# Kernel optimization log

Hardware: AMD Instinct MI355X
Metric: run time of the kernel (lower is better)

The kernel has to match this reference:

```python
import jax, jax.numpy as jnp
import numpy as np

K = 20

def knn_idx(x, k):
    # x: [N, D] -> indices of k nearest neighbors (excluding self), [N, k]
    sq = jnp.sum(x * x, axis=-1)
    d = sq[:, None] + sq[None, :] - 2.0 * (x @ x.T)
    n = x.shape[0]
    d = d.at[jnp.arange(n), jnp.arange(n)].set(jnp.inf)
    _, idx = jax.lax.top_k(-d, k)
    return idx

def edge_conv(x, W, b, k):
    # DynamicEdgeConv: feat = [x_i, x_j - x_i] -> MLP -> max over neighbors
    idx = knn_idx(x, k)                      # [N, k]
    xj = x[idx]                              # [N, k, D]
    xi = jnp.broadcast_to(x[:, None, :], xj.shape)
    feat = jnp.concatenate([xi, xj - xi], axis=-1)   # [N, k, 2D]
    h = jax.nn.relu(feat @ W + b)            # [N, k, C]
    return jnp.max(h, axis=1)                # [N, C]

def dilate_flat(x, W, b, k):
    # DilateFlatEdgeConv: flat morphological dilation (max over kNN) + MLP
    idx = knn_idx(x, k)
    dil = jnp.max(x[idx], axis=1)            # [N, C]
    return jax.nn.relu(dil @ W + b)

def setup_inputs() -> dict:
    key = jax.random.key(0)
    ks = jax.random.split(key, 12)
    N, C, NC = 8192, 64, 16
    s = 0.05
    return {
        "x": jax.random.normal(ks[0], (N, 3), dtype=jnp.float32),
        "W1": jax.random.normal(ks[1], (6, C), dtype=jnp.float32) * s,
        "b1": jnp.zeros((C,), jnp.float32),
        "Wd1": jax.random.normal(ks[2], (C, C), dtype=jnp.float32) * s,
        "bd1": jnp.zeros((C,), jnp.float32),
        "Wd2": jax.random.normal(ks[3], (C, C), dtype=jnp.float32) * s,
        "bd2": jnp.zeros((C,), jnp.float32),
        "Wd3": jax.random.normal(ks[4], (C, C), dtype=jnp.float32) * s,
        "bd3": jnp.zeros((C,), jnp.float32),
        "Wl": jax.random.normal(ks[5], (3 * C, 1024), dtype=jnp.float32) * s,
        "bl": jnp.zeros((1024,), jnp.float32),
        "Wm1": jax.random.normal(ks[6], (1024, 256), dtype=jnp.float32) * s,
        "bm1": jnp.zeros((256,), jnp.float32),
        "Wm2": jax.random.normal(ks[7], (256, 128), dtype=jnp.float32) * s,
        "bm2": jnp.zeros((128,), jnp.float32),
        "Wm3": jax.random.normal(ks[8], (128, NC), dtype=jnp.float32) * s,
        "bm3": jnp.zeros((NC,), jnp.float32),
    }

def reference(x, W1, b1, Wd1, bd1, Wd2, bd2, Wd3, bd3, Wl, bl, Wm1, bm1, Wm2, bm2, Wm3, bm3):
    x_feat = edge_conv(x, W1, b1, K)          # [N, 64]
    x1 = dilate_flat(x_feat, Wd1, bd1, K) - x_feat
    x2 = dilate_flat(x1, Wd2, bd2, K) - x1
    x3 = dilate_flat(x2, Wd3, bd3, K) - x2
    h = jax.nn.relu(jnp.concatenate([x1, x2, x3], axis=1) @ Wl + bl)  # [N, 1024]
    h = jax.nn.relu(h @ Wm1 + bm1)            # dropout is identity at eval
    h = jax.nn.relu(h @ Wm2 + bm2)
    logits = h @ Wm3 + bm3
    return jax.nn.log_softmax(logits, axis=-1)
```

## Files before the change

### kernel.cpp

```cpp
#include <hip/hip_runtime.h>
#include <math.h>

#define NPTS 8192
#define KNN 20
#define KSEL 8
#define CAPD3 256
#define CAP64 512
#define LCAP 2048

typedef __attribute__((ext_vector_type(8))) short bf16x8;
typedef __attribute__((ext_vector_type(16))) float f32x16;

__device__ __forceinline__ uint32_t fkey(float v) {
  uint32_t b = __float_as_uint(v);
  return b ^ ((uint32_t)((int)b >> 31) | 0x80000000u);
}
__device__ __forceinline__ float unkey(uint32_t k) {
  uint32_t b = (k & 0x80000000u) ? (k ^ 0x80000000u) : ~k;
  return __uint_as_float(b);
}
__device__ __forceinline__ ushort f2bf(float v) {
  uint32_t u = __float_as_uint(v);
  u += 0x7FFFu + ((u >> 16) & 1u);
  return (ushort)(u >> 16);
}
__device__ __forceinline__ float bf2f(ushort h) {
  return __uint_as_float(((uint32_t)h) << 16);
}

__device__ __forceinline__ void insert8k(uint32_t (&d)[KSEL], uint32_t key) {
#pragma unroll
  for (int r = 0; r < KSEL; ++r) {
    uint32_t nd = min(d[r], key);
    key = max(d[r], key);
    d[r] = nd;
  }
}

__global__ void sqnorm_kernel(const float* __restrict__ x, int ldx, int D,
                              float* __restrict__ sq,
                              unsigned int* __restrict__ nmax2u) {
  int i = blockIdx.x * blockDim.x + threadIdx.x;
  if (i >= NPTS) return;
  const float* xr = x + (size_t)i * ldx;
  float s = 0.f;
  for (int d = 0; d < D; ++d) { float v = xr[d]; s += v * v; }
  sq[i] = s;
  atomicMax(nmax2u, __float_as_uint(s));
}

__global__ __launch_bounds__(256) void tobf16_kernel(
    const float* __restrict__ x, int ldx, ushort* __restrict__ xh,
    ushort* __restrict__ xl) {
  const int i = blockIdx.x * 256 + threadIdx.x;
  const int row = (i * 8) >> 6, col = (i * 8) & 63;
  const float* src = &x[(size_t)row * ldx + col];
  ushort oh[8], ol[8];
#pragma unroll
  for (int e = 0; e < 8; ++e) {
    float v = src[e];
    ushort h = f2bf(v);
    oh[e] = h;
    ol[e] = f2bf(v - bf2f(h));
  }
  *(ushort4*)&xh[(size_t)row * 64 + col] =
      make_ushort4(oh[0], oh[1], oh[2], oh[3]);
  *(ushort4*)&xh[(size_t)row * 64 + col + 4] =
      make_ushort4(oh[4], oh[5], oh[6], oh[7]);
  *(ushort4*)&xl[(size_t)row * 64 + col] =
      make_ushort4(ol[0], ol[1], ol[2], ol[3]);
  *(ushort4*)&xl[(size_t)row * 64 + col + 4] =
      make_ushort4(ol[4], ol[5], ol[6], ol[7]);
}

#define WRITE_S(QR, BASE)                                                   \
  {                                                                         \
    const int cc = (4 * bg) & 31;                                           \
    const int jbase = cb + (QR)*32 + cc;                                    \
    _Pragma("unroll") for (int u = 0; u < 8; ++u) {                         \
      const int row = 4 * am + (u & 3) + 64 * (u >> 2);                     \
      const int gq = qb * 128 + row;                                        \
      const int sw = ((row & 7) ^ ((row >> 2) & 7)) << 2;                   \
      uint32_t k0 = fkey(fmaf(-2.f, acc[u][(BASE) + 0], sc[(BASE) + 0]));   \
      uint32_t k1 = fkey(fmaf(-2.f, acc[u][(BASE) + 1], sc[(BASE) + 1]));   \
      uint32_t k2 = fkey(fmaf(-2.f, acc[u][(BASE) + 2], sc[(BASE) + 2]));   \
      uint32_t k3 = fkey(fmaf(-2.f, acc[u][(BASE) + 3], sc[(BASE) + 3]));   \
      if (jbase + 0 == gq) k0 = 0xFFFFFFFFu;                                \
      if (jbase + 1 == gq) k1 = 0xFFFFFFFFu;                                \
      if (jbase + 2 == gq) k2 = 0xFFFFFFFFu;                                \
      if (jbase + 3 == gq) k3 = 0xFFFFFFFFu;                                \
      *(uint4*)&S[row * 32 + (cc ^ sw)] = make_uint4(k0, k1, k2, k3);       \
    }                                                                       \
  }

#define COMMIT_CS()                                                         \
  {                                                                         \
    Cs[(ck + 0) * 128 + cn] = p0.x;  Cs[(ck + 1) * 128 + cn] = p0.y;        \
    Cs[(ck + 2) * 128 + cn] = p0.z;  Cs[(ck + 3) * 128 + cn] = p0.w;        \
    Cs[(ck + 4) * 128 + cn] = p1.x;  Cs[(ck + 5) * 128 + cn] = p1.y;        \
    Cs[(ck + 6) * 128 + cn] = p1.z;  Cs[(ck + 7) * 128 + cn] = p1.w;        \
    Cs[(ck + 8) * 128 + cn] = p2.x;  Cs[(ck + 9) * 128 + cn] = p2.y;        \
    Cs[(ck + 10) * 128 + cn] = p2.z; Cs[(ck + 11) * 128 + cn] = p2.w;       \
    Cs[(ck + 12) * 128 + cn] = p3.x; Cs[(ck + 13) * 128 + cn] = p3.y;       \
    Cs[(ck + 14) * 128 + cn] = p3.z; Cs[(ck + 15) * 128 + cn] = p3.w;       \
  }

#define ISSUE_CS(BASEROW, KOFF)                                             \
  {                                                                         \
    const float* src_ = &x[(size_t)((BASEROW) + cn) * LDX + (KOFF) + ck];   \
    p0 = *(const float4*)&src_[0];                                          \
    p1 = *(const float4*)&src_[4];                                          \
    p2 = *(const float4*)&src_[8];                                          \
    p3 = *(const float4*)&src_[12];                                         \
  }

template <int LDX>
__global__ __launch_bounds__(256, 2) void knn_gemm_kernel(
    const float* __restrict__ x, const float* __restrict__ sq,
    uint32_t* __restrict__ pk) {
  __shared__ float Qs[64 * 128];
  __shared__ uint32_t CsS[32 * 128];
  float* const Cs = (float*)CsS;
  uint32_t* const S = CsS;
  const int t = threadIdx.x;
  const int qb = blockIdx.x;
  const int ch = blockIdx.y;
  const int am = t & 15;
  const int bg = (t >> 4) & 15;
  const int cn = t & 127;
  const int ck = (t >> 7) * 16;

  {
    const int q = t & 127;
    const int k0 = (t >> 7) * 32;
    const float* src = &x[(size_t)(qb * 128 + q) * LDX + k0];
#pragma unroll
    for (int c = 0; c < 8; ++c) {
      float4 v = *(const float4*)&src[c * 4];
      Qs[(k0 + c * 4 + 0) * 128 + q] = v.x;
      Qs[(k0 + c * 4 + 1) * 128 + q] = v.y;
      Qs[(k0 + c * 4 + 2) * 128 + q] = v.z;
      Qs[(k0 + c * 4 + 3) * 128 + q] = v.w;
    }
  }

  const int selq = t & 127, part = t >> 7;
  uint32_t dreg[KSEL];
#pragma unroll
  for (int r = 0; r < KSEL; ++r) dreg[r] = 0xFFFFFFFFu;

  float4 p0, p1, p2, p3;
  ISSUE_CS(ch * 256, 0)

#pragma unroll 1
  for (int tile = 0; tile < 2; ++tile) {
    const int cb = ch * 256 + tile * 128;
    float acc[8][8] = {};
#pragma unroll
    for (int kh = 0; kh < 2; ++kh) {
      __syncthreads();
      COMMIT_CS()
      if (kh == 0) {
        ISSUE_CS(cb, 32)
      } else if (tile == 0) {
        ISSUE_CS(cb + 128, 0)
      }
      __syncthreads();
#pragma unroll 4
      for (int k2 = 0; k2 < 32; ++k2) {
        const int k = kh * 32 + k2;
        float4 A0 = *(const float4*)&Qs[k * 128 + 4 * am];
        float4 A1 = *(const float4*)&Qs[k * 128 + 4 * am + 64];
        float4 B0 = *(const float4*)&Cs[k2 * 128 + 4 * bg];
        float4 B1 = *(const float4*)&Cs[k2 * 128 + 4 * bg + 64];
        float a[8] = {A0.x, A0.y, A0.z, A0.w, A1.x, A1.y, A1.z, A1.w};
        float b[8] = {B0.x, B0.y, B0.z, B0.w, B1.x, B1.y, B1.z, B1.w};
#pragma unroll
        for (int u = 0; u < 8; ++u)
#pragma unroll
          for (int v = 0; v < 8; ++v) acc[u][v] = fmaf(a[u], b[v], acc[u][v]);
      }
    }
    float4 s0 = *(const float4*)&sq[cb + 4 * bg];
    float4 s1 = *(const float4*)&sq[cb + 4 * bg + 64];
    float sc[8] = {s0.x, s0.y, s0.z, s0.w, s1.x, s1.y, s1.z, s1.w};

    const int qlow = bg >> 3;
    for (int qr = 0; qr < 4; ++qr) {
      __syncthreads();
      if (qr == qlow) WRITE_S(qr, 0);
      if (qr == 2 + qlow) WRITE_S(qr, 4);
      __syncthreads();
      const int swr = ((selq & 7) ^ ((selq >> 2) & 7)) << 2;
#pragma unroll
      for (int g_ = 0; g_ < 4; ++g_) {
        const int cc = part * 16 + g_ * 4;
        uint4 sv = *(const uint4*)&S[selq * 32 + (cc ^ swr)];
        uint32_t kv[4] = {sv.x, sv.y, sv.z, sv.w};
#pragma unroll
        for (int e = 0; e < 4; ++e) {
          if (kv[e] < dreg[KSEL - 1]) insert8k(dreg, kv[e]);
        }
      }
    }
  }
  const int l = ch * 2 + part;
  uint32_t* pkq = pk + ((size_t)l * NPTS + (qb * 128 + selq)) * KSEL;
#pragma unroll
  for (int r = 0; r < KSEL; ++r) pkq[r] = dreg[r];
}

__global__ __launch_bounds__(256) void knn_mergeT_kernel(
    const uint32_t* __restrict__ pk, const float* __restrict__ sq,
    const float* __restrict__ nmax2, float* __restrict__ Tf, float mscale) {
  __shared__ uint32_t sk[16][16][KSEL];
  const int t = threadIdx.x;
  const int ql = t >> 4;
  const int l = t & 15;
  const int q = blockIdx.x * 16 + ql;
  const uint32_t* pkq = pk + ((size_t)l * NPTS + q) * KSEL;
#pragma unroll
  for (int r = 0; r < KSEL; ++r) sk[ql][l][r] = pkq[r];
  __syncthreads();
  int ptr = 0;
  uint32_t k = 0;
#pragma unroll 1
  for (int s = 0; s < KNN; ++s) {
    k = (ptr < KSEL) ? sk[ql][l][ptr] : 0xFFFFFFFFu;
    int src = l;
#pragma unroll
    for (int off = 8; off >= 1; off >>= 1) {
      uint32_t ok = __shfl_xor(k, off, 16);
      int osrc = __shfl_xor(src, off, 16);
      bool take = (ok < k) || (ok == k && osrc < src);
      k = take ? ok : k;
      src = take ? osrc : src;
    }
    if (l == src) ptr++;
  }
  if (l == 0) Tf[q] = unkey(k) + mscale * sqrtf(sq[q] * nmax2[0]);
}

__global__ __launch_bounds__(256, 2) void knn_recover_mfma_kernel(
    const ushort* __restrict__ xh, const ushort* __restrict__ xl,
    const float* __restrict__ sq, const float* __restrict__ Tf,
    uint32_t* __restrict__ cnt, int* __restrict__ cj) {
  __shared__ uint32_t nsurv;
  __shared__ uint2 surv[LCAP];
  const int t = threadIdx.x;
  const int w = t >> 6, l = t & 63;
  const int q0 = blockIdx.x * 128 + (w >> 1) * 64;
  const int c0 = blockIdx.y * 128 + (w & 1) * 64;
  const int lr = l & 31;
  const int ko = (l >> 5) * 8;
  const int rowbase = (l >> 5) * 4;

  if (t == 0) nsurv = 0;

  float tq[2][16];
#pragma unroll
  for (int rt = 0; rt < 2; ++rt)
#pragma unroll
    for (int r = 0; r < 16; ++r)
      tq[rt][r] = Tf[q0 + rt * 32 + (r & 3) + 8 * (r >> 2) + rowbase];

  f32x16 acc[2][2] = {};
#pragma unroll
  for (int kk = 0; kk < 4; ++kk) {
    bf16x8 Ah[2], Al[2], Bh[2], Bl[2];
#pragma unroll
    for (int rt = 0; rt < 2; ++rt) {
      const size_t off = (size_t)(q0 + rt * 32 + lr) * 64 + kk * 16 + ko;
      Ah[rt] = *(const bf16x8*)&xh[off];
      Al[rt] = *(const bf16x8*)&xl[off];
    }
#pragma unroll
    for (int ct = 0; ct < 2; ++ct) {
      const size_t off = (size_t)(c0 + ct * 32 + lr) * 64 + kk * 16 + ko;
      Bh[ct] = *(const bf16x8*)&xh[off];
      Bl[ct] = *(const bf16x8*)&xl[off];
    }
#pragma unroll
    for (int rt = 0; rt < 2; ++rt)
#pragma unroll
      for (int ct = 0; ct < 2; ++ct) {
        acc[rt][ct] = __builtin_amdgcn_mfma_f32_32x32x16_bf16(
            Ah[rt], Bh[ct], acc[rt][ct], 0, 0, 0);
        acc[rt][ct] = __builtin_amdgcn_mfma_f32_32x32x16_bf16(
            Ah[rt], Bl[ct], acc[rt][ct], 0, 0, 0);
        acc[rt][ct] = __builtin_amdgcn_mfma_f32_32x32x16_bf16(
            Al[rt], Bh[ct], acc[rt][ct], 0, 0, 0);
      }
  }
  __syncthreads();

#pragma unroll
  for (int ct = 0; ct < 2; ++ct) {
    const int j = c0 + ct * 32 + lr;
    const float sqj = sq[j];
#pragma unroll
    for (int rt = 0; rt < 2; ++rt) {
#pragma unroll
      for (int r = 0; r < 16; ++r) {
        const int gq = q0 + rt * 32 + (r & 3) + 8 * (r >> 2) + rowbase;
        float d = fmaf(-2.f, acc[rt][ct][r], sqj);
        if (j != gq && d <= tq[rt][r]) {
          uint32_t idx = atomicAdd(&nsurv, 1u);
          if (idx < (uint32_t)LCAP) {
            surv[idx] = make_uint2((uint32_t)gq, (uint32_t)j);
          } else {
            uint32_t slot = atomicAdd(&cnt[gq], 1u);
            if (slot < (uint32_t)CAP64) cj[(size_t)gq * CAP64 + slot] = j;
          }
        }
      }
    }
  }
  __syncthreads();
  const uint32_t nv = min(nsurv, (uint32_t)LCAP);
#pragma unroll 1
  for (uint32_t i = t; i < nv; i += 256) {
    uint2 e = surv[i];
    uint32_t slot = atomicAdd(&cnt[e.x], 1u);
    if (slot < (uint32_t)CAP64) cj[(size_t)e.x * CAP64 + slot] = (int)e.y;
  }
}

template <int LDX>
__global__ __launch_bounds__(256) void knn_final64_kernel(
    const float* __restrict__ x, const float* __restrict__ sq,
    const uint32_t* __restrict__ cnt, const int* __restrict__ cj,
    int* __restrict__ idx_out) {
  __shared__ float xqs[4][64];
  const int t = threadIdx.x, w = t >> 6, l = t & 63;
  const int q = blockIdx.x * 4 + w;
  if (l < 16)
    *(float4*)&xqs[w][l * 4] = *(const float4*)&x[(size_t)q * LDX + l * 4];
  __syncthreads();
  const int n = (int)min(cnt[q], (uint32_t)CAP64);
  uint32_t ks[8]; int js[8];
#pragma unroll
  for (int r = 0; r < 8; ++r) { ks[r] = 0xFFFFFFFFu; js[r] = 0x7fffffff; }
#pragma unroll 1
  for (int it = 0; it < 8; ++it) {
    const int c = l + it * 64;
    if (c < n) {
      const int j = cj[(size_t)q * CAP64 + c];
      const float* xj = &x[(size_t)j * LDX];
      float dot = 0.f;
#pragma unroll
      for (int e = 0; e < 16; ++e) {
        float4 a = *(const float4*)&xj[e * 4];
        float4 b = *(const float4*)&xqs[w][e * 4];
        dot = fmaf(a.x, b.x, dot);
        dot = fmaf(a.y, b.y, dot);
        dot = fmaf(a.z, b.z, dot);
        dot = fmaf(a.w, b.w, dot);
      }
      float d = fmaf(-2.f, dot, sq[j]);
      uint32_t ck = fkey(d);
      int ci = j;
#pragma unroll
      for (int r = 0; r < 8; ++r) {
        bool sw = (ck < ks[r]) || (ck == ks[r] && ci < js[r]);
        uint32_t ok = ks[r]; int oj = js[r];
        ks[r] = sw ? ck : ok; js[r] = sw ? ci : oj;
        ck = sw ? ok : ck; ci = sw ? oj : ci;
      }
    }
  }
#pragma unroll 1
  for (int s = 0; s < KNN; ++s) {
    uint32_t mk = ks[0];
    int mj = js[0];
#pragma unroll
    for (int off = 32; off >= 1; off >>= 1) {
      uint32_t ok = __shfl_xor(mk, off, 64);
      int oj = __shfl_xor(mj, off, 64);
      bool take = (ok < mk) || (ok == mk && oj < mj);
      mk = take ? ok : mk;
      mj = take ? oj : mj;
    }
    if (ks[0] == mk && js[0] == mj) {
#pragma unroll
      for (int r = 0; r < 7; ++r) { ks[r] = ks[r + 1]; js[r] = js[r + 1]; }
      ks[7] = 0xFFFFFFFFu; js[7] = 0x7fffffff;
    }
    if (l == 0) idx_out[(size_t)q * KNN + s] = mj;
  }
}

__global__ __launch_bounds__(256) void knn_d3k_kernel(
    const float* __restrict__ x, const float* __restrict__ sq,
    uint32_t* __restrict__ pk) {
  __shared__ float4 Ct[128];
  const int t = threadIdx.x;
  const int q = blockIdx.x * 256 + t;
  const int ch = blockIdx.y;
  const int cb = ch * 128;
  if (t < 128)
    Ct[t] = make_float4(x[(cb + t) * 3], x[(cb + t) * 3 + 1],
                        x[(cb + t) * 3 + 2], sq[cb + t]);
  const float xi0 = x[q * 3], xi1 = x[q * 3 + 1], xi2 = x[q * 3 + 2];
  uint32_t dreg[KSEL];
#pragma unroll
  for (int r = 0; r < KSEL; ++r) dreg[r] = 0xFFFFFFFFu;
  __syncthreads();
#pragma unroll 1
  for (int c = 0; c < 128; ++c) {
    float4 cv = Ct[c];
    int j = cb + c;
    float val = fmaf(-2.f, xi0 * cv.x + xi1 * cv.y + xi2 * cv.z, cv.w);
    uint32_t key = fkey(val);
    if (j != q && key < dreg[KSEL - 1]) insert8k(dreg, key);
  }
  uint32_t* pkq = pk + ((size_t)ch * NPTS + q) * KSEL;
#pragma unroll
  for (int r = 0; r < KSEL; ++r) pkq[r] = dreg[r];
}

__global__ __launch_bounds__(256) void knn_d3_recover_kernel(
    const float* __restrict__ x, const float* __restrict__ sq,
    const float* __restrict__ Tf, uint32_t* __restrict__ cnt,
    uint32_t* __restrict__ cd, int* __restrict__ cj) {
  __shared__ float4 Ct[256];
  const int t = threadIdx.x;
  const int q = blockIdx.x * 256 + t;
  const int ch = blockIdx.y;
  const int cb = ch * 256;
  Ct[t] = make_float4(x[(cb + t) * 3], x[(cb + t) * 3 + 1],
                      x[(cb + t) * 3 + 2], sq[cb + t]);
  const float xi0 = x[q * 3], xi1 = x[q * 3 + 1], xi2 = x[q * 3 + 2];
  const float Tq = Tf[q];
  __syncthreads();
#pragma unroll 1
  for (int c = 0; c < 256; ++c) {
    float4 cv = Ct[c];
    int j = cb + c;
    float val = fmaf(-2.f, xi0 * cv.x + xi1 * cv.y + xi2 * cv.z, cv.w);
    if (j != q && val <= Tq) {
      uint32_t slot = atomicAdd(&cnt[q], 1u);
      if (slot < (uint32_t)CAPD3) {
        cd[(size_t)q * CAPD3 + slot] = fkey(val);
        cj[(size_t)q * CAPD3 + slot] = j;
      }
    }
  }
}

#define CSWAP(ka, ja, kb, jb)                                   \
  {                                                             \
    bool sw = (kb < ka) || (kb == ka && jb < ja);               \
    uint32_t tk = sw ? kb : ka; int tj = sw ? jb : ja;          \
    kb = sw ? ka : kb; jb = sw ? ja : jb;                       \
    ka = tk; ja = tj;                                           \
  }

__global__ __launch_bounds__(256) void knn_final_d3_kernel(
    const uint32_t* __restrict__ cnt, const uint32_t* __restrict__ cd,
    const int* __restrict__ cj, int* __restrict__ idx_out) {
  const int t = threadIdx.x;
  const int w = t >> 6;
  const int l = t & 63;
  const int q = blockIdx.x * 4 + w;
  const int n = (int)min(cnt[q], (uint32_t)CAPD3);
  uint32_t k0 = 0xFFFFFFFFu, k1 = 0xFFFFFFFFu, k2 = 0xFFFFFFFFu,
           k3 = 0xFFFFFFFFu;
  int j0 = 0x7fffffff, j1 = 0x7fffffff, j2 = 0x7fffffff, j3 = 0x7fffffff;
  if (l < n) { k0 = cd[(size_t)q * CAPD3 + l]; j0 = cj[(size_t)q * CAPD3 + l]; }
  if (l + 64 < n) { k1 = cd[(size_t)q * CAPD3 + l + 64]; j1 = cj[(size_t)q * CAPD3 + l + 64]; }
  if (l + 128 < n) { k2 = cd[(size_t)q * CAPD3 + l + 128]; j2 = cj[(size_t)q * CAPD3 + l + 128]; }
  if (l + 192 < n) { k3 = cd[(size_t)q * CAPD3 + l + 192]; j3 = cj[(size_t)q * CAPD3 + l + 192]; }
  CSWAP(k0, j0, k1, j1); CSWAP(k2, j2, k3, j3);
  CSWAP(k0, j0, k2, j2); CSWAP(k1, j1, k3, j3);
  CSWAP(k1, j1, k2, j2);
#pragma unroll 1
  for (int s = 0; s < KNN; ++s) {
    uint32_t mk = k0;
    int mj = j0;
#pragma unroll
    for (int off = 32; off >= 1; off >>= 1) {
      uint32_t ok = __shfl_xor(mk, off, 64);
      int oj = __shfl_xor(mj, off, 64);
      bool take = (ok < mk) || (ok == mk && oj < mj);
      mk = take ? ok : mk;
      mj = take ? oj : mj;
    }
    if (k0 == mk && j0 == mj) {
      k0 = k1; j0 = j1; k1 = k2; j1 = j2; k2 = k3; j2 = j3;
      k3 = 0xFFFFFFFFu; j3 = 0x7fffffff;
    }
    if (l == 0) idx_out[(size_t)q * KNN + s] = mj;
  }
}

__global__ __launch_bounds__(256) void edgeconv_kernel(
    const float* __restrict__ x, const int* __restrict__ idx,
    const float* __restrict__ W1, const float* __restrict__ b1,
    float* __restrict__ out) {
  const int i = blockIdx.x * 4 + (threadIdx.x >> 6);
  const int c = threadIdx.x & 63;
  float w0 = W1[c], w1 = W1[64 + c], w2 = W1[128 + c];
  float w3 = W1[192 + c], w4 = W1[256 + c], w5 = W1[320 + c];
  float xi0 = x[3 * i], xi1 = x[3 * i + 1], xi2 = x[3 * i + 2];
  float base = b1[c] + xi0 * w0 + xi1 * w1 + xi2 * w2;
  float m = -INFINITY;
#pragma unroll
  for (int k = 0; k < KNN; ++k) {
    int j = idx[i * KNN + k];
    float d0 = x[3 * j] - xi0, d1 = x[3 * j + 1] - xi1, d2 = x[3 * j + 2] - xi2;
    float h = base + d0 * w3 + d1 * w4 + d2 * w5;
    m = fmaxf(m, fmaxf(h, 0.f));
  }
  out[(size_t)i * 64 + c] = m;
}

__global__ __launch_bounds__(256) void dilate_kernel(
    const float* __restrict__ xin, int ldin, const int* __restrict__ idx,
    const float* __restrict__ W, const float* __restrict__ bias,
    float* __restrict__ out, int ldout) {
  const int g = threadIdx.x >> 6;
  const int i = blockIdx.x * 4 + g;
  const int c = threadIdx.x & 63;
  __shared__ float dil[4][64];
  float m = -INFINITY;
#pragma unroll
  for (int k = 0; k < KNN; ++k) {
    int j = idx[i * KNN + k];
    m = fmaxf(m, xin[(size_t)j * ldin + c]);
  }
  dil[g][c] = m;
  __syncthreads();
  float acc = bias[c];
#pragma unroll
  for (int d = 0; d < 64; ++d) acc = fmaf(dil[g][d], W[d * 64 + c], acc);
  out[(size_t)i * ldout + c] = fmaxf(acc, 0.f) - xin[(size_t)i * ldin + c];
}

template <int BN>
__global__ __launch_bounds__(256) void gemm128_kernel(
    const float* __restrict__ A, int K, int ldA, const float* __restrict__ W,
    int N, const float* __restrict__ bias, float* __restrict__ C, int ldC,
    int relu) {
  constexpr int VN = BN / 16;
  __shared__ float As[16 * 128];
  __shared__ float Bs[16 * BN];
  const int t = threadIdx.x;
  const int bn = blockIdx.x * BN;
  const int bm = blockIdx.y * 128;
  const int am = t & 15;
  const int bg = (t >> 4) & 15;
  float acc[8][VN] = {};

  for (int k0 = 0; k0 < K; k0 += 16) {
    __syncthreads();
    {
      const int m = t & 127;
      const int ka = (t >> 7) * 8;
      const float* src = &A[(size_t)(bm + m) * ldA + k0 + ka];
      float4 v0 = *(const float4*)&src[0];
      float4 v1 = *(const float4*)&src[4];
      As[(ka + 0) * 128 + m] = v0.x;
      As[(ka + 1) * 128 + m] = v0.y;
      As[(ka + 2) * 128 + m] = v0.z;
      As[(ka + 3) * 128 + m] = v0.w;
      As[(ka + 4) * 128 + m] = v1.x;
      As[(ka + 5) * 128 + m] = v1.y;
      As[(ka + 6) * 128 + m] = v1.z;
      As[(ka + 7) * 128 + m] = v1.w;
    }
    if constexpr (BN == 128) {
      const int kb = t >> 4;
      const int n8 = (t & 15) * 8;
      const float* src = &W[(size_t)(k0 + kb) * N + bn + n8];
      float4 v0 = *(const float4*)&src[0];
      float4 v1 = *(const float4*)&src[4];
      *(float4*)&Bs[kb * BN + n8] = v0;
      *(float4*)&Bs[kb * BN + n8 + 4] = v1;
    } else {
      const int kb = t >> 4;
      const int n4 = (t & 15) * 4;
      const float* src = &W[(size_t)(k0 + kb) * N + bn + n4];
      *(float4*)&Bs[kb * BN + n4] = *(const float4*)&src[0];
    }
    __syncthreads();
#pragma unroll
    for (int k = 0; k < 16; ++k) {
      float4 A0 = *(const float4*)&As[k * 128 + 4 * am];
      float4 A1 = *(const float4*)&As[k * 128 + 4 * am + 64];
      float a[8] = {A0.x, A0.y, A0.z, A0.w, A1.x, A1.y, A1.z, A1.w};
      float b[VN];
      float4 B0 = *(const float4*)&Bs[k * BN + 4 * bg];
      b[0] = B0.x; b[1] = B0.y; b[2] = B0.z; b[3] = B0.w;
      if constexpr (BN == 128) {
        float4 B1 = *(const float4*)&Bs[k * BN + 4 * bg + 64];
        b[4] = B1.x; b[5] = B1.y; b[6] = B1.z; b[7] = B1.w;
      }
#pragma unroll
      for (int u = 0; u < 8; ++u)
#pragma unroll
        for (int v = 0; v < VN; ++v) acc[u][v] = fmaf(a[u], b[v], acc[u][v]);
    }
  }
#pragma unroll
  for (int u = 0; u < 8; ++u) {
    const int m = bm + 4 * am + (u & 3) + 64 * (u >> 2);
#pragma unroll
    for (int vq = 0; vq < VN / 4; ++vq) {
      const int n = bn + 4 * bg + 64 * vq;
      float4 o;
      float* po = (float*)&o;
#pragma unroll
      for (int e = 0; e < 4; ++e) {
        float val = acc[u][vq * 4 + e] + bias[n + e];
        po[e] = relu ? fmaxf(val, 0.f) : val;
      }
      *(float4*)&C[(size_t)m * ldC + n] = o;
    }
  }
}

__global__ __launch_bounds__(256) void final_kernel(
    const float* __restrict__ h3, const float* __restrict__ Wm3,
    const float* __restrict__ bm3, float* __restrict__ out) {
  __shared__ float hs[16][132];
  const int tid = threadIdx.x;
  const int r = tid >> 4, c = tid & 15;
  const int row0 = blockIdx.x * 16;
#pragma unroll
  for (int l = tid; l < 2048; l += 256)
    hs[l >> 7][l & 127] = h3[(size_t)row0 * 128 + l];
  __syncthreads();
  float acc = bm3[c];
#pragma unroll
  for (int d = 0; d < 128; ++d) acc = fmaf(hs[r][d], Wm3[d * 16 + c], acc);
  float mx = acc;
#pragma unroll
  for (int o = 8; o >= 1; o >>= 1) mx = fmaxf(mx, __shfl_xor(mx, o, 16));
  float e = expf(acc - mx);
  float s = e;
#pragma unroll
  for (int o = 8; o >= 1; o >>= 1) s += __shfl_xor(s, o, 16);
  out[(size_t)(row0 + r) * 16 + c] = (acc - mx) - logf(s);
}

extern "C" void kernel_launch(void* const* d_in, const int* in_sizes, int n_in,
                              void* d_out, int out_size, void* d_ws,
                              size_t ws_size, hipStream_t stream) {
  const float* x = (const float*)d_in[0];
  const float* W1 = (const float*)d_in[1];
  const float* b1 = (const float*)d_in[2];
  const float* Wd1 = (const float*)d_in[3];
  const float* bd1 = (const float*)d_in[4];
  const float* Wd2 = (const float*)d_in[5];
  const float* bd2 = (const float*)d_in[6];
  const float* Wd3 = (const float*)d_in[7];
  const float* bd3 = (const float*)d_in[8];
  const float* Wl = (const float*)d_in[9];
  const float* bl = (const float*)d_in[10];
  const float* Wm1 = (const float*)d_in[11];
  const float* bm1 = (const float*)d_in[12];
  const float* Wm2 = (const float*)d_in[13];
  const float* bm2 = (const float*)d_in[14];
  const float* Wm3 = (const float*)d_in[15];
  const float* bm3 = (const float*)d_in[16];
  float* out = (float*)d_out;

  char* ws = (char*)d_ws;
  float* sq = (float*)(ws + 0);
  int* idxA = (int*)(ws + 32768);
  float* xfeat = (float*)(ws + 1343488);
  float* xcat = (float*)(ws + 3440640);
  float* h1 = (float*)(ws + 9732096);
  float* h2 = (float*)(ws + 43286528);
  float* h3 = (float*)(ws + 51675136);
  float* x1 = xcat;
  float* x2 = xcat + 64;
  float* x3 = xcat + 128;
  uint32_t* pk = (uint32_t*)(ws + 9732096);
  uint32_t* cdD3 = (uint32_t*)(ws + 13926400);
  int* cjD3 = (int*)(ws + 22315008);
  float* Tf = (float*)(ws + 30703616);
  uint32_t* cnt = (uint32_t*)(ws + 30736384);
  unsigned int* nmax2u = (unsigned int*)(ws + 30769152);
  float* nmax2f = (float*)nmax2u;
  int* cj64 = (int*)(ws + 30769216);
  ushort* xh = (ushort*)(ws + 47546432);
  ushort* xl = (ushort*)(ws + 48595008);

  hipMemsetAsync(cnt, 0, 32768 + 64, stream);
  sqnorm_kernel<<<32, 256, 0, stream>>>(x, 3, 3, sq, nmax2u);
  knn_d3k_kernel<<<dim3(32, 16), 256, 0, stream>>>(x, sq, pk);
  knn_mergeT_kernel<<<NPTS / 16, 256, 0, stream>>>(pk, sq, nmax2f, Tf, 0.f);
  knn_d3_recover_kernel<<<dim3(32, 32), 256, 0, stream>>>(x, sq, Tf, cnt,
                                                          cdD3, cjD3);
  knn_final_d3_kernel<<<NPTS / 4, 256, 0, stream>>>(cnt, cdD3, cjD3, idxA);
  edgeconv_kernel<<<NPTS / 4, 256, 0, stream>>>(x, idxA, W1, b1, xfeat);

#define KNN64_PASS(XIN, LDX)                                                  \
  hipMemsetAsync(cnt, 0, 32768 + 64, stream);                                 \
  sqnorm_kernel<<<32, 256, 0, stream>>>(XIN, LDX, 64, sq, nmax2u);            \
  tobf16_kernel<<<256, 256, 0, stream>>>(XIN, LDX, xh, xl);                   \
  knn_gemm_kernel<LDX><<<dim3(64, 8), 256, 0, stream>>>(XIN, sq, pk);         \
  knn_mergeT_kernel<<<NPTS / 16, 256, 0, stream>>>(pk, sq, nmax2f, Tf,        \
                                                   1e-4f);                    \
  knn_recover_mfma_kernel<<<dim3(64, 64), 256, 0, stream>>>(xh, xl, sq, Tf,   \
                                                            cnt, cj64);       \
  knn_final64_kernel<LDX><<<NPTS / 4, 256, 0, stream>>>(XIN, sq, cnt, cj64,   \
                                                        idxA);

  KNN64_PASS(xfeat, 64)
  dilate_kernel<<<NPTS / 4, 256, 0, stream>>>(xfeat, 64, idxA, Wd1, bd1, x1,
                                              192);
  KNN64_PASS(x1, 192)
  dilate_kernel<<<NPTS / 4, 256, 0, stream>>>(x1, 192, idxA, Wd2, bd2, x2,
                                              192);
  KNN64_PASS(x2, 192)
  dilate_kernel<<<NPTS / 4, 256, 0, stream>>>(x2, 192, idxA, Wd3, bd3, x3,
                                              192);
#undef KNN64_PASS

  gemm128_kernel<128><<<dim3(1024 / 128, NPTS / 128), 256, 0, stream>>>(
      xcat, 192, 192, Wl, 1024, bl, h1, 1024, 1);
  gemm128_kernel<64><<<dim3(256 / 64, NPTS / 128), 256, 0, stream>>>(
      h1, 1024, 1024, Wm1, 256, bm1, h2, 256, 1);
  gemm128_kernel<64><<<dim3(128 / 64, NPTS / 128), 256, 0, stream>>>(
      h2, 256, 256, Wm2, 128, bm2, h3, 128, 1);
  final_kernel<<<NPTS / 16, 256, 0, stream>>>(h3, Wm3, bm3, out);
}
```

Baseline: 1.013 ms.

## Stage kNN recover survivors in LDS and prefetch GEMM tiles into registers

The d3 recover kernel now collects threshold survivors in a shared-memory list through an LDS atomic, then flushes them to global per-query buckets after a barrier. This replaces per-hit global atomics issued inside the divergent scan loop; entries that overflow the shared list still take the old global path. Separately, the fp32 GEMM kernel now loads the next K-tile's A and B values into registers while the current tile is computed, overlapping global loads with FMA work at the cost of extra registers.

```diff
diff --git a/kernel.cpp b/kernel.cpp
--- a/kernel.cpp
+++ b/kernel.cpp
@@ -424,10 +424,13 @@
     const float* __restrict__ Tf, uint32_t* __restrict__ cnt,
     uint32_t* __restrict__ cd, int* __restrict__ cj) {
   __shared__ float4 Ct[256];
+  __shared__ uint32_t nsurv;
+  __shared__ uint2 surv[LCAP];
   const int t = threadIdx.x;
-  const int q = blockIdx.x * 256 + t;
-  const int ch = blockIdx.y;
-  const int cb = ch * 256;
+  const int q0 = blockIdx.x * 256;
+  const int q = q0 + t;
+  const int cb = blockIdx.y * 256;
+  if (t == 0) nsurv = 0;
   Ct[t] = make_float4(x[(cb + t) * 3], x[(cb + t) * 3 + 1],
                       x[(cb + t) * 3 + 2], sq[cb + t]);
   const float xi0 = x[q * 3], xi1 = x[q * 3 + 1], xi2 = x[q * 3 + 2];
@@ -439,11 +442,29 @@
     int j = cb + c;
     float val = fmaf(-2.f, xi0 * cv.x + xi1 * cv.y + xi2 * cv.z, cv.w);
     if (j != q && val <= Tq) {
-      uint32_t slot = atomicAdd(&cnt[q], 1u);
-      if (slot < (uint32_t)CAPD3) {
-        cd[(size_t)q * CAPD3 + slot] = fkey(val);
-        cj[(size_t)q * CAPD3 + slot] = j;
-      }
+      uint32_t idx = atomicAdd(&nsurv, 1u);
+      if (idx < (uint32_t)LCAP) {
+        surv[idx] = make_uint2(fkey(val), ((uint32_t)t << 16) | (uint32_t)j);
+      } else {
+        uint32_t slot = atomicAdd(&cnt[q], 1u);
+        if (slot < (uint32_t)CAPD3) {
+          cd[(size_t)q * CAPD3 + slot] = fkey(val);
+          cj[(size_t)q * CAPD3 + slot] = j;
+        }
+      }
+    }
+  }
+  __syncthreads();
+  const uint32_t nv = min(nsurv, (uint32_t)LCAP);
+#pragma unroll 1
+  for (uint32_t i = t; i < nv; i += 256) {
+    uint2 e = surv[i];
+    const int qq = q0 + (int)(e.y >> 16);
+    const int jj = (int)(e.y & 0xFFFFu);
+    uint32_t slot = atomicAdd(&cnt[qq], 1u);
+    if (slot < (uint32_t)CAPD3) {
+      cd[(size_t)qq * CAPD3 + slot] = e.x;
+      cj[(size_t)qq * CAPD3 + slot] = jj;
     }
   }
 }
@@ -550,38 +571,41 @@
   const int bm = blockIdx.y * 128;
   const int am = t & 15;
   const int bg = (t >> 4) & 15;
+  const int m_ = t & 127;
+  const int ka = (t >> 7) * 8;
+  const int kb = t >> 4;
+  const int nb = (t & 15) * (BN == 128 ? 8 : 4);
   float acc[8][VN] = {};
+  float4 av0, av1, bv0, bv1;
+
+  {
+    const float* srcA = &A[(size_t)(bm + m_) * ldA + ka];
+    av0 = *(const float4*)&srcA[0];
+    av1 = *(const float4*)&srcA[4];
+    const float* srcB = &W[(size_t)kb * N + bn + nb];
+    bv0 = *(const float4*)&srcB[0];
+    if constexpr (BN == 128) bv1 = *(const float4*)&srcB[4];
+  }
 
   for (int k0 = 0; k0 < K; k0 += 16) {
     __syncthreads();
-    {
-      const int m = t & 127;
-      const int ka = (t >> 7) * 8;
-      const float* src = &A[(size_t)(bm + m) * ldA + k0 + ka];
-      float4 v0 = *(const float4*)&src[0];
-      float4 v1 = *(const float4*)&src[4];
-      As[(ka + 0) * 128 + m] = v0.x;
-      As[(ka + 1) * 128 + m] = v0.y;
-      As[(ka + 2) * 128 + m] = v0.z;
-      As[(ka + 3) * 128 + m] = v0.w;
-      As[(ka + 4) * 128 + m] = v1.x;
-      As[(ka + 5) * 128 + m] = v1.y;
-      As[(ka + 6) * 128 + m] = v1.z;
-      As[(ka + 7) * 128 + m] = v1.w;
-    }
-    if constexpr (BN == 128) {
-      const int kb = t >> 4;
-      const int n8 = (t & 15) * 8;
-      const float* src = &W[(size_t)(k0 + kb) * N + bn + n8];
-      float4 v0 = *(const float4*)&src[0];
-      float4 v1 = *(const float4*)&src[4];
-      *(float4*)&Bs[kb * BN + n8] = v0;
-      *(float4*)&Bs[kb * BN + n8 + 4] = v1;
-    } else {
-      const int kb = t >> 4;
-      const int n4 = (t & 15) * 4;
-      const float* src = &W[(size_t)(k0 + kb) * N + bn + n4];
-      *(float4*)&Bs[kb * BN + n4] = *(const float4*)&src[0];
+    As[(ka + 0) * 128 + m_] = av0.x;
+    As[(ka + 1) * 128 + m_] = av0.y;
+    As[(ka + 2) * 128 + m_] = av0.z;
+    As[(ka + 3) * 128 + m_] = av0.w;
+    As[(ka + 4) * 128 + m_] = av1.x;
+    As[(ka + 5) * 128 + m_] = av1.y;
+    As[(ka + 6) * 128 + m_] = av1.z;
+    As[(ka + 7) * 128 + m_] = av1.w;
+    *(float4*)&Bs[kb * BN + nb] = bv0;
+    if constexpr (BN == 128) *(float4*)&Bs[kb * BN + nb + 4] = bv1;
+    if (k0 + 16 < K) {
+      const float* srcA = &A[(size_t)(bm + m_) * ldA + k0 + 16 + ka];
+      av0 = *(const float4*)&srcA[0];
+      av1 = *(const float4*)&srcA[4];
+      const float* srcB = &W[(size_t)(k0 + 16 + kb) * N + bn + nb];
+      bv0 = *(const float4*)&srcB[0];
+      if constexpr (BN == 128) bv1 = *(const float4*)&srcB[4];
     }
     __syncthreads();
 #pragma unroll
```

Result: faster. 915.8 us (median of 2 runs) (-9.6%).
